# Kernel optimization log

Measured on AMD Instinct MI355X. Metric: run time of the kernel, lower is better.

Reference implementation:

```python
import jax, jax.numpy as jnp
import numpy as np

B, P, N, De, H, Do, T = 256, 48, 64, 64, 128, 64, 5
NR = N * (N - 1)
EPS = 1e-5


def _w(k, o, i):
    return jax.random.normal(k, (o, i), jnp.float32) * (1.0 / np.sqrt(i))


def setup_inputs() -> dict:
    key = jax.random.key(0)
    ks = jax.random.split(key, 12)
    x = jax.random.normal(ks[0], (B, P, N), jnp.float32)
    # fully-connected directed edges without self-loops (order matches itertools.product)
    idx = np.array([(r, s) for r in range(N) for s in range(N) if r != s], dtype=np.int32)
    receivers = jnp.asarray(idx[:, 0])
    senders = jnp.asarray(idx[:, 1])
    inp = {
        "x": x,
        "receivers": receivers,
        "senders": senders,
        "bn_gamma": jnp.ones((P,), jnp.float32),
        "bn_beta": jnp.zeros((P,), jnp.float32),
        "fr1_w": _w(ks[1], 4 * De, 2 * P), "fr1_b": jnp.zeros((4 * De,), jnp.float32),
        "fr2_w": _w(ks[2], 2 * De, 4 * De), "fr2_b": jnp.zeros((2 * De,), jnp.float32),
        "fr3_w": _w(ks[3], De, 2 * De), "fr3_b": jnp.zeros((De,), jnp.float32),
        "fo1_w": _w(ks[4], 2 * H, P + De), "fo1_b": jnp.zeros((2 * H,), jnp.float32),
        "fo2_w": _w(ks[5], H, 2 * H), "fo2_b": jnp.zeros((H,), jnp.float32),
        "fo3_w": _w(ks[6], Do, H), "fo3_b": jnp.zeros((Do,), jnp.float32),
        "fc1_w": _w(ks[7], 5 * T, Do), "fc1_b": jnp.zeros((5 * T,), jnp.float32),
        "fc2_w": _w(ks[8], 3 * T, 5 * T), "fc2_b": jnp.zeros((3 * T,), jnp.float32),
        "fc3_w": _w(ks[9], T, 3 * T), "fc3_b": jnp.zeros((T,), jnp.float32),
    }
    return inp


def _conv1(x, w, b):  # 1x1 Conv1d: x [B,Cin,L], w [Cout,Cin]
    return jnp.einsum('oi,bil->bol', w, x) + b[None, :, None]


def _forward(x, receivers, senders, bn_gamma, bn_beta,
             fr1_w, fr1_b, fr2_w, fr2_b, fr3_w, fr3_b,
             fo1_w, fo1_b, fo2_w, fo2_b, fo3_w, fo3_b,
             fc1_w, fc1_b, fc2_w, fc2_b, fc3_w, fc3_b):
    relu = jax.nn.relu
    # BatchNorm1d(P) in training mode: stats over (batch, length)
    mean = jnp.mean(x, axis=(0, 2), keepdims=True)
    var = jnp.var(x, axis=(0, 2), keepdims=True)
    xn = (x - mean) * jax.lax.rsqrt(var + EPS)
    xn = xn * bn_gamma[None, :, None] + bn_beta[None, :, None]
    # tmul(x, Rr)/tmul(x, Rs) are one-hot gathers along node axis -> [B, P, Nr]
    Orr = xn[:, :, receivers]
    Ors = xn[:, :, senders]
    Bmat = jnp.concatenate([Orr, Ors], axis=1)  # [B, 2P, Nr]
    Bmat = relu(_conv1(Bmat, fr1_w, fr1_b))
    Bmat = relu(_conv1(Bmat, fr2_w, fr2_b))
    E = relu(_conv1(Bmat, fr3_w, fr3_b))  # [B, De, Nr]
    # tmul(E, Rr^T) is scatter-add of edge features onto receiver nodes
    Ebar = jnp.zeros((x.shape[0], De, N), E.dtype).at[:, :, receivers].add(E)
    C = jnp.concatenate([xn, Ebar], axis=1)  # [B, P+De, N]
    C = relu(_conv1(C, fo1_w, fo1_b))
    C = relu(_conv1(C, fo2_w, fo2_b))
    O = relu(_conv1(C, fo3_w, fo3_b))  # [B, Do, N]
    Nsum = jnp.sum(O, axis=2)  # sum over constituents -> [B, Do]
    # fc_fixed1/2/3 applied with NO intermediate activations
    out = Nsum @ fc1_w.T + fc1_b
    out = out @ fc2_w.T + fc2_b
    out = out @ fc3_w.T + fc3_b
    return out


def reference(x, receivers, senders, bn_gamma, bn_beta,
              fr1_w, fr1_b, fr2_w, fr2_b, fr3_w, fr3_b,
              fo1_w, fo1_b, fo2_w, fo2_b, fo3_w, fo3_b,
              fc1_w, fc1_b, fc2_w, fc2_b, fc3_w, fc3_b):
    return _forward(x, receivers, senders, bn_gamma, bn_beta,
                    fr1_w, fr1_b, fr2_w, fr2_b, fr3_w, fr3_b,
                    fo1_w, fo1_b, fo2_w, fo2_b, fo3_w, fo3_b,
                    fc1_w, fc1_b, fc2_w, fc2_b, fc3_w, fc3_b)
```

## Files before the change

kernel.cpp:

```cpp
#include <hip/hip_runtime.h>
#include <hip/hip_bf16.h>

#define BB 256
#define PP 48
#define NN 64
#define EPSBN 1e-5f

typedef __attribute__((ext_vector_type(8))) short bf16x8;
typedef __attribute__((ext_vector_type(4))) float f32x4;

#define BIGO 0
#define S1SO 32768
#define S1RO 49152
#define F3LO 65536
#define A2WO 73728
#define XNTP 73728
#define B2LO 81408
#define REDO 81664
#define LDSE 81920

#define W_FR1R 0
#define W_FR1S 16384
#define W_FR2  32768
#define W_FR3  65536
#define W_FO1  73728
#define W_FO2  106496
#define W_FO3  139264
#define W_TOT  147456

union U8 { bf16x8 v; unsigned u[4]; };

__device__ __forceinline__ unsigned pku(float a, float b) {
    union { __hip_bfloat162 h; unsigned u; } cv;
    cv.h = __float22bfloat162_rn(make_float2(a, b));
    return cv.u;
}
__device__ __forceinline__ ushort f2b(float f) {
    union { float f; unsigned u; } a; a.f = f;
    unsigned u = a.u + 0x7FFFu + ((a.u >> 16) & 1u);
    return (ushort)(u >> 16);
}
__device__ __forceinline__ float loF(unsigned u) { union { unsigned x; float f; } c; c.x = u << 16; return c.f; }
__device__ __forceinline__ float hiF(unsigned u) { union { unsigned x; float f; } c; c.x = u & 0xffff0000u; return c.f; }

__device__ __forceinline__ int sidx(int row, int k, int kpad) {
    return row * kpad + ((((k >> 3) ^ (row & 7)) << 3) | (k & 7));
}
__device__ __forceinline__ bf16x8 ldfrag(const ushort* buf, int row, int k, int kpad) {
    return *(const bf16x8*)(buf + row * kpad + (((k >> 3) ^ (row & 7)) << 3));
}
__device__ __forceinline__ bf16x8 ldfrag40(const ushort* buf, int row, int k) {
    return *(const bf16x8*)(buf + row * 40 + k);
}
__device__ __forceinline__ f32x4 MFMA(bf16x8 a, bf16x8 b, f32x4 c) {
    return __builtin_amdgcn_mfma_f32_16x16x32_bf16(a, b, c, 0, 0, 0);
}
__device__ __forceinline__ void stAct(ushort* buf, int row, int c0, int kpad, f32x4 a, float4 bi) {
    uint2 o;
    o.x = pku(fmaxf(a[0] + bi.x, 0.f), fmaxf(a[1] + bi.y, 0.f));
    o.y = pku(fmaxf(a[2] + bi.z, 0.f), fmaxf(a[3] + bi.w, 0.f));
    *(uint2*)(buf + row * kpad + ((((c0 >> 3) ^ (row & 7)) << 3) | (c0 & 7))) = o;
}
__device__ __forceinline__ void stAct040(ushort* buf, int row, int c0, f32x4 a) {
    uint2 o;
    o.x = pku(fmaxf(a[0], 0.f), fmaxf(a[1], 0.f));
    o.y = pku(fmaxf(a[2], 0.f), fmaxf(a[3], 0.f));
    *(uint2*)(buf + row * 40 + c0) = o;
}
__device__ __forceinline__ void stRaw(ushort* buf, int row, int c0, int kpad, f32x4 a, float4 bi) {
    uint2 o;
    o.x = pku(a[0] + bi.x, a[1] + bi.y);
    o.y = pku(a[2] + bi.z, a[3] + bi.w);
    *(uint2*)(buf + row * kpad + ((((c0 >> 3) ^ (row & 7)) << 3) | (c0 & 7))) = o;
}

__global__ __launch_bounds__(256) void bn_stats_kernel(
    const float* __restrict__ x, const float* __restrict__ gamma,
    const float* __restrict__ beta, float* __restrict__ scale, float* __restrict__ bias)
{
    __shared__ float s_sum[256], s_sq[256];
    int p = blockIdx.x, t = threadIdx.x;
    float sum = 0.f, sq = 0.f;
    for (int i = t; i < BB * NN; i += 256) {
        int b = i >> 6, n = i & 63;
        float v = x[b * PP * NN + p * NN + n];
        sum += v; sq += v * v;
    }
    s_sum[t] = sum; s_sq[t] = sq;
    __syncthreads();
    for (int off = 128; off > 0; off >>= 1) {
        if (t < off) { s_sum[t] += s_sum[t + off]; s_sq[t] += s_sq[t + off]; }
        __syncthreads();
    }
    if (t == 0) {
        float inv = 1.f / (float)(BB * NN);
        float mean = s_sum[0] * inv;
        float var  = s_sq[0] * inv - mean * mean;
        float sc   = gamma[p] * rsqrtf(var + EPSBN);
        scale[p] = sc;
        bias[p]  = beta[p] - mean * sc;
    }
}

__global__ __launch_bounds__(512) void prep_kernel(
    const float* __restrict__ fr1_w, const float* __restrict__ fr2_w,
    const float* __restrict__ fr3_w, const float* __restrict__ fo1_w,
    const float* __restrict__ fo2_w, const float* __restrict__ fo3_w,
    ushort* __restrict__ wsw)
{
    int i = blockIdx.x * 512 + threadIdx.x;
    if (i >= W_TOT) return;
    float v; int off, row, k, kpad;
    if (i < 16384)        { row = i >> 6; k = i & 63; kpad = 64;  off = W_FR1R;
                            v = (k < PP) ? fr1_w[row * 96 + k] : 0.f; }
    else if (i < 32768)   { int j = i - 16384;  row = j >> 6; k = j & 63;  kpad = 64;  off = W_FR1S;
                            v = (k < PP) ? fr1_w[row * 96 + PP + k] : 0.f; }
    else if (i < 65536)   { int j = i - 32768;  row = j >> 8; k = j & 255; kpad = 256; off = W_FR2;
                            v = fr2_w[row * 256 + k]; }
    else if (i < 73728)   { int j = i - 65536;  row = j >> 7; k = j & 127; kpad = 128; off = W_FR3;
                            v = fr3_w[row * 128 + k]; }
    else if (i < 106496)  { int j = i - 73728;  row = j >> 7; k = j & 127; kpad = 128; off = W_FO1;
                            v = (k < 64) ? fo1_w[row * 112 + PP + k]
                              : (k < 112 ? fo1_w[row * 112 + (k - 64)] : 0.f); }
    else if (i < 139264)  { int j = i - 106496; row = j >> 8; k = j & 255; kpad = 256; off = W_FO2;
                            v = fo2_w[row * 256 + k]; }
    else                  { int j = i - 139264; row = j >> 7; k = j & 127; kpad = 128; off = W_FO3;
                            v = fo3_w[row * 128 + k]; }
    wsw[off + sidx(row, k, kpad)] = f2b(v);
}

__device__ __forceinline__ void wcopy(ushort* dst, const ushort* src, int n, int t) {
    for (int i = t * 8; i < n; i += 768 * 8)
        *(uint4*)(dst + i) = *(const uint4*)(src + i);
}

__global__ __launch_bounds__(768, 3) void meg_kernel(
    const float* __restrict__ x,
    const float* __restrict__ scl, const float* __restrict__ bia,
    const ushort* __restrict__ wsw,
    const float* __restrict__ fr1_b, const float* __restrict__ fr2_b,
    const float* __restrict__ fr3_b, const float* __restrict__ fo1_b,
    const float* __restrict__ fo2_b, const float* __restrict__ fo3_b,
    const float* __restrict__ fc1_w, const float* __restrict__ fc1_b,
    const float* __restrict__ fc2_w, const float* __restrict__ fc2_b,
    const float* __restrict__ fc3_w, const float* __restrict__ fc3_b,
    float* __restrict__ out)
{
    __shared__ __align__(16) ushort L[LDSE];

    int b = blockIdx.x, t = threadIdx.x;
    int w = t >> 6, l = t & 63, lx = l & 15, lq = l >> 4;

    for (int i = t; i < 4096; i += 768) {
        int n = i & 63, k = i >> 6;
        float v = (k < PP) ? x[b * PP * NN + k * NN + n] * scl[k] + bia[k] : 0.f;
        L[XNTP + sidx(n, k, 64)] = f2b(v);
    }
    wcopy(L + BIGO,         wsw + W_FR1R, 16384, t);
    wcopy(L + BIGO + 16384, wsw + W_FR1S, 16384, t);
    wcopy(L + F3LO,         wsw + W_FR3,  8192, t);
    if (t < 128) ((float*)(L + B2LO))[t] = fr2_b[t];
    __syncthreads();

    for (int mt = w; mt < 16; mt += 12) {
        f32x4 aR[4], aS[4];
#pragma unroll
        for (int nt = 0; nt < 4; ++nt) { aR[nt] = (f32x4){0.f,0.f,0.f,0.f}; aS[nt] = (f32x4){0.f,0.f,0.f,0.f}; }
#pragma unroll
        for (int ks = 0; ks < 2; ++ks) {
            bf16x8 AfR = ldfrag(L + BIGO,         mt * 16 + lx, ks * 32 + lq * 8, 64);
            bf16x8 AfS = ldfrag(L + BIGO + 16384, mt * 16 + lx, ks * 32 + lq * 8, 64);
#pragma unroll
            for (int nt = 0; nt < 4; ++nt) {
                bf16x8 Bf = ldfrag(L + XNTP, nt * 16 + lx, ks * 32 + lq * 8, 64);
                aR[nt] = MFMA(AfR, Bf, aR[nt]);
                aS[nt] = MFMA(AfS, Bf, aS[nt]);
            }
        }
        int ch0 = mt * 16 + lq * 4;
        float4 bi = *(const float4*)(fr1_b + ch0);
        float4 zb = make_float4(0.f, 0.f, 0.f, 0.f);
#pragma unroll
        for (int nt = 0; nt < 4; ++nt) {
            stRaw(L + S1RO, nt * 16 + lx, ch0, 256, aR[nt], bi);
            stRaw(L + S1SO, nt * 16 + lx, ch0, 256, aS[nt], zb);
        }
    }
    __syncthreads();

    wcopy(L + BIGO, wsw + W_FR2, 32768, t);
    float b3c[4];
#pragma unroll
    for (int n3 = 0; n3 < 4; ++n3) b3c[n3] = fr3_b[n3 * 16 + lx];
    __syncthreads();

    ushort* a2w = L + A2WO + w * 640;
    const float* b2L = (const float*)(L + B2LO);
#pragma unroll 1
    for (int r = w; r < 64; r += 12) {
        float part[4] = {0.f, 0.f, 0.f, 0.f};
#pragma unroll 1
        for (int p = 0; p < 2; ++p) {
            int eA = p * 32 + lx, eB = eA + 16;
            int sA = eA + (eA >= r);
            int sB = eB + (eB >= r); if (sB > 63) sB = 63;

            f32x4 acc2[8][2];
#pragma unroll
            for (int m = 0; m < 8; ++m) {
                float4 bv = *(const float4*)(b2L + m * 16 + lq * 4);
                f32x4 bi; bi[0] = bv.x; bi[1] = bv.y; bi[2] = bv.z; bi[3] = bv.w;
                acc2[m][0] = bi; acc2[m][1] = bi;
            }
#pragma unroll
            for (int ks = 0; ks < 8; ++ks) {
                int ko = ks * 32 + lq * 8;
                U8 fr, fa, fb;
                fr.v = ldfrag(L + S1RO, r,  ko, 256);
                fa.v = ldfrag(L + S1SO, sA, ko, 256);
                fb.v = ldfrag(L + S1SO, sB, ko, 256);
                U8 bA, bB;
#pragma unroll
                for (int jj = 0; jj < 4; ++jj) {
                    float r0 = loF(fr.u[jj]), r1 = hiF(fr.u[jj]);
                    bA.u[jj] = pku(fmaxf(r0 + loF(fa.u[jj]), 0.f), fmaxf(r1 + hiF(fa.u[jj]), 0.f));
                    bB.u[jj] = pku(fmaxf(r0 + loF(fb.u[jj]), 0.f), fmaxf(r1 + hiF(fb.u[jj]), 0.f));
                }
#pragma unroll
                for (int m = 0; m < 8; ++m) {
                    bf16x8 Af = ldfrag(L + BIGO, m * 16 + lx, ko, 256);
                    acc2[m][0] = MFMA(Af, bA.v, acc2[m][0]);
                    acc2[m][1] = MFMA(Af, bB.v, acc2[m][1]);
                }
            }
            f32x4 acc3[2][4];
#pragma unroll
            for (int cc = 0; cc < 2; ++cc)
#pragma unroll
                for (int n3 = 0; n3 < 4; ++n3) acc3[cc][n3] = (f32x4){0.f,0.f,0.f,0.f};
#pragma unroll
            for (int h = 0; h < 4; ++h) {
                bf16x8 bW[4];
#pragma unroll
                for (int n3 = 0; n3 < 4; ++n3)
                    bW[n3] = ldfrag(L + F3LO, n3 * 16 + lx, h * 32 + lq * 8, 128);
#pragma unroll
                for (int cc = 0; cc < 2; ++cc) {
                    stAct040(a2w, lx, lq * 4,      acc2[2 * h][cc]);
                    stAct040(a2w, lx, 16 + lq * 4, acc2[2 * h + 1][cc]);
                    bf16x8 af = ldfrag40(a2w, lx, lq * 8);
#pragma unroll
                    for (int n3 = 0; n3 < 4; ++n3)
                        acc3[cc][n3] = MFMA(af, bW[n3], acc3[cc][n3]);
                }
            }
#pragma unroll
            for (int cc = 0; cc < 2; ++cc) {
                bool mpad = (p == 1) && (cc == 1) && (lq == 3);
#pragma unroll
                for (int n3 = 0; n3 < 4; ++n3) {
                    float bv = b3c[n3];
                    float s = fmaxf(acc3[cc][n3][0] + bv, 0.f) + fmaxf(acc3[cc][n3][1] + bv, 0.f)
                            + fmaxf(acc3[cc][n3][2] + bv, 0.f);
                    float s3 = fmaxf(acc3[cc][n3][3] + bv, 0.f);
                    part[n3] += s + (mpad ? 0.f : s3);
                }
            }
        }
#pragma unroll
        for (int n3 = 0; n3 < 4; ++n3) {
            part[n3] += __shfl_xor(part[n3], 16, 64);
            part[n3] += __shfl_xor(part[n3], 32, 64);
        }
        if (lq == 0) {
#pragma unroll
            for (int n3 = 0; n3 < 4; ++n3)
                L[S1RO + sidx(r, n3 * 16 + lx, 256)] = f2b(part[n3]);
        }
    }
    __syncthreads();

    wcopy(L + BIGO, wsw + W_FO1, 32768, t);
    for (int i = t; i < 4096; i += 768) {
        int n = i & 63, k = i >> 6;
        float v = (k < PP) ? x[b * PP * NN + k * NN + n] * scl[k] + bia[k] : 0.f;
        L[S1RO + sidx(n, 64 + k, 256)] = f2b(v);
    }
    __syncthreads();

    for (int mt = w; mt < 16; mt += 12) {
        f32x4 accN[4];
#pragma unroll
        for (int nt = 0; nt < 4; ++nt) accN[nt] = (f32x4){0.f,0.f,0.f,0.f};
#pragma unroll
        for (int ks = 0; ks < 4; ++ks) {
            bf16x8 Af = ldfrag(L + BIGO, mt * 16 + lx, ks * 32 + lq * 8, 128);
#pragma unroll
            for (int nt = 0; nt < 4; ++nt) {
                bf16x8 Bf = ldfrag(L + S1RO, nt * 16 + lx, ks * 32 + lq * 8, 256);
                accN[nt] = MFMA(Af, Bf, accN[nt]);
            }
        }
        int ch0 = mt * 16 + lq * 4;
        float4 bi = *(const float4*)(fo1_b + ch0);
#pragma unroll
        for (int nt = 0; nt < 4; ++nt)
            stAct(L + S1SO, nt * 16 + lx, ch0, 256, accN[nt], bi);
    }
    __syncthreads();

    wcopy(L + BIGO, wsw + W_FO2, 32768, t);
    wcopy(L + S1RO, wsw + W_FO3, 8192, t);
    __syncthreads();

    if (w < 8) {
        f32x4 a2N[4];
#pragma unroll
        for (int nt = 0; nt < 4; ++nt) a2N[nt] = (f32x4){0.f,0.f,0.f,0.f};
#pragma unroll
        for (int ks = 0; ks < 8; ++ks) {
            bf16x8 Af = ldfrag(L + BIGO, w * 16 + lx, ks * 32 + lq * 8, 256);
#pragma unroll
            for (int nt = 0; nt < 4; ++nt) {
                bf16x8 Bf = ldfrag(L + S1SO, nt * 16 + lx, ks * 32 + lq * 8, 256);
                a2N[nt] = MFMA(Af, Bf, a2N[nt]);
            }
        }
        int ch0 = w * 16 + lq * 4;
        float4 bi = *(const float4*)(fo2_b + ch0);
#pragma unroll
        for (int nt = 0; nt < 4; ++nt)
            stAct(L + F3LO, nt * 16 + lx, ch0, 128, a2N[nt], bi);
    }
    __syncthreads();

    if (w < 4) {
        f32x4 a3N[4];
#pragma unroll
        for (int nt = 0; nt < 4; ++nt) a3N[nt] = (f32x4){0.f,0.f,0.f,0.f};
#pragma unroll
        for (int ks3 = 0; ks3 < 4; ++ks3) {
            bf16x8 Af = ldfrag(L + S1RO, 16 * w + lx, ks3 * 32 + lq * 8, 128);
#pragma unroll
            for (int nt = 0; nt < 4; ++nt) {
                bf16x8 Bf = ldfrag(L + F3LO, nt * 16 + lx, ks3 * 32 + lq * 8, 128);
                a3N[nt] = MFMA(Af, Bf, a3N[nt]);
            }
        }
        float4 b3 = *(const float4*)(fo3_b + 16 * w + lq * 4);
        float o0 = 0.f, o1 = 0.f, o2 = 0.f, o3 = 0.f;
#pragma unroll
        for (int nt = 0; nt < 4; ++nt) {
            o0 += fmaxf(a3N[nt][0] + b3.x, 0.f);
            o1 += fmaxf(a3N[nt][1] + b3.y, 0.f);
            o2 += fmaxf(a3N[nt][2] + b3.z, 0.f);
            o3 += fmaxf(a3N[nt][3] + b3.w, 0.f);
        }
#pragma unroll
        for (int off = 8; off >= 1; off >>= 1) {
            o0 += __shfl_xor(o0, off, 16);
            o1 += __shfl_xor(o1, off, 16);
            o2 += __shfl_xor(o2, off, 16);
            o3 += __shfl_xor(o3, off, 16);
        }
        if (lx == 0) {
            float* red = (float*)(L + REDO);
            *(float4*)&red[16 * w + lq * 4] = make_float4(o0, o1, o2, o3);
        }
    }
    __syncthreads();

    {
        float* red = (float*)(L + REDO);
        float* h1  = red + 64;
        float* h2  = red + 96;
        if (t < 25) {
            float s = fc1_b[t];
            for (int k = 0; k < 64; ++k) s += fc1_w[t * 64 + k] * red[k];
            h1[t] = s;
        }
        __syncthreads();
        if (t < 15) {
            float s = fc2_b[t];
            for (int k = 0; k < 25; ++k) s += fc2_w[t * 25 + k] * h1[k];
            h2[t] = s;
        }
        __syncthreads();
        if (t < 5) {
            float s = fc3_b[t];
            for (int k = 0; k < 15; ++k) s += fc3_w[t * 15 + k] * h2[k];
            out[b * 5 + t] = s;
        }
    }
}

extern "C" void kernel_launch(void* const* d_in, const int* in_sizes, int n_in,
                              void* d_out, int out_size, void* d_ws, size_t ws_size,
                              hipStream_t stream)
{
    const float* x        = (const float*)d_in[0];
    const float* bn_gamma = (const float*)d_in[3];
    const float* bn_beta  = (const float*)d_in[4];
    const float* fr1_w = (const float*)d_in[5];
    const float* fr1_b = (const float*)d_in[6];
    const float* fr2_w = (const float*)d_in[7];
    const float* fr2_b = (const float*)d_in[8];
    const float* fr3_w = (const float*)d_in[9];
    const float* fr3_b = (const float*)d_in[10];
    const float* fo1_w = (const float*)d_in[11];
    const float* fo1_b = (const float*)d_in[12];
    const float* fo2_w = (const float*)d_in[13];
    const float* fo2_b = (const float*)d_in[14];
    const float* fo3_w = (const float*)d_in[15];
    const float* fo3_b = (const float*)d_in[16];
    const float* fc1_w = (const float*)d_in[17];
    const float* fc1_b = (const float*)d_in[18];
    const float* fc2_w = (const float*)d_in[19];
    const float* fc2_b = (const float*)d_in[20];
    const float* fc3_w = (const float*)d_in[21];
    const float* fc3_b = (const float*)d_in[22];

    float* ws    = (float*)d_ws;
    float* scale = ws;
    float* bias  = ws + 64;
    ushort* wsw  = (ushort*)(ws + 128);
    float* out   = (float*)d_out;

    bn_stats_kernel<<<dim3(PP), dim3(256), 0, stream>>>(x, bn_gamma, bn_beta, scale, bias);
    prep_kernel<<<dim3(W_TOT / 512), dim3(512), 0, stream>>>(
        fr1_w, fr2_w, fr3_w, fo1_w, fo2_w, fo3_w, wsw);
    meg_kernel<<<dim3(BB), dim3(768), 0, stream>>>(
        x, scale, bias, wsw,
        fr1_b, fr2_b, fr3_b, fo1_b, fo2_b, fo3_b,
        fc1_w, fc1_b, fc2_w, fc2_b, fc3_w, fc3_b, out);
}
```

Baseline: 231.7 us.

## Precompute normalized bf16 swizzled input in prep kernel and parallelize FC tail

The batch-normalized, transposed, bf16-swizzled input is now produced once per batch element in the prep kernel and stored in the workspace. The main kernel pulls it in with vectorized 16-byte copies instead of doing strided fp32 gathers and conversion twice. The fo1 GEMM reads its x-part straight from that buffer rather than first copying it into the S1RO region. BN stats now runs 1024 threads per block, and the final three tiny FC layers use wave-level shuffle reductions instead of a few serial threads, at the cost of an extra 2 MB workspace round-trip.

```diff
diff --git a/kernel.cpp b/kernel.cpp
--- a/kernel.cpp
+++ b/kernel.cpp
@@ -27,6 +27,8 @@
 #define W_FO2  106496
 #define W_FO3  139264
 #define W_TOT  147456
+#define W_XNT  147456
+#define W_ALL  (W_XNT + BB * 4096)
 
 union U8 { bf16x8 v; unsigned u[4]; };
 
@@ -74,21 +76,21 @@
     *(uint2*)(buf + row * kpad + ((((c0 >> 3) ^ (row & 7)) << 3) | (c0 & 7))) = o;
 }
 
-__global__ __launch_bounds__(256) void bn_stats_kernel(
+__global__ __launch_bounds__(1024) void bn_stats_kernel(
     const float* __restrict__ x, const float* __restrict__ gamma,
     const float* __restrict__ beta, float* __restrict__ scale, float* __restrict__ bias)
 {
-    __shared__ float s_sum[256], s_sq[256];
+    __shared__ float s_sum[1024], s_sq[1024];
     int p = blockIdx.x, t = threadIdx.x;
     float sum = 0.f, sq = 0.f;
-    for (int i = t; i < BB * NN; i += 256) {
+    for (int i = t; i < BB * NN; i += 1024) {
         int b = i >> 6, n = i & 63;
         float v = x[b * PP * NN + p * NN + n];
         sum += v; sq += v * v;
     }
     s_sum[t] = sum; s_sq[t] = sq;
     __syncthreads();
-    for (int off = 128; off > 0; off >>= 1) {
+    for (int off = 512; off > 0; off >>= 1) {
         if (t < off) { s_sum[t] += s_sum[t + off]; s_sq[t] += s_sq[t + off]; }
         __syncthreads();
     }
@@ -106,10 +108,18 @@
     const float* __restrict__ fr1_w, const float* __restrict__ fr2_w,
     const float* __restrict__ fr3_w, const float* __restrict__ fo1_w,
     const float* __restrict__ fo2_w, const float* __restrict__ fo3_w,
-    ushort* __restrict__ wsw)
+    const float* __restrict__ x, const float* __restrict__ scale,
+    const float* __restrict__ bias, ushort* __restrict__ wsw)
 {
     int i = blockIdx.x * 512 + threadIdx.x;
-    if (i >= W_TOT) return;
+    if (i >= W_ALL) return;
+    if (i >= W_TOT) {
+        int j = i - W_XNT;
+        int b = j >> 12, nk = j & 4095, n = nk & 63, k = nk >> 6;
+        float v = (k < PP) ? x[b * PP * NN + k * NN + n] * scale[k] + bias[k] : 0.f;
+        wsw[W_XNT + (b << 12) + sidx(n, k, 64)] = f2b(v);
+        return;
+    }
     float v; int off, row, k, kpad;
     if (i < 16384)        { row = i >> 6; k = i & 63; kpad = 64;  off = W_FR1R;
                             v = (k < PP) ? fr1_w[row * 96 + k] : 0.f; }
@@ -135,8 +145,6 @@
 }
 
 __global__ __launch_bounds__(768, 3) void meg_kernel(
-    const float* __restrict__ x,
-    const float* __restrict__ scl, const float* __restrict__ bia,
     const ushort* __restrict__ wsw,
     const float* __restrict__ fr1_b, const float* __restrict__ fr2_b,
     const float* __restrict__ fr3_b, const float* __restrict__ fo1_b,
@@ -151,11 +159,7 @@
     int b = blockIdx.x, t = threadIdx.x;
     int w = t >> 6, l = t & 63, lx = l & 15, lq = l >> 4;
 
-    for (int i = t; i < 4096; i += 768) {
-        int n = i & 63, k = i >> 6;
-        float v = (k < PP) ? x[b * PP * NN + k * NN + n] * scl[k] + bia[k] : 0.f;
-        L[XNTP + sidx(n, k, 64)] = f2b(v);
-    }
+    wcopy(L + XNTP,         wsw + W_XNT + (b << 12), 4096, t);
     wcopy(L + BIGO,         wsw + W_FR1R, 16384, t);
     wcopy(L + BIGO + 16384, wsw + W_FR1S, 16384, t);
     wcopy(L + F3LO,         wsw + W_FR3,  8192, t);
@@ -281,11 +285,7 @@
     __syncthreads();
 
     wcopy(L + BIGO, wsw + W_FO1, 32768, t);
-    for (int i = t; i < 4096; i += 768) {
-        int n = i & 63, k = i >> 6;
-        float v = (k < PP) ? x[b * PP * NN + k * NN + n] * scl[k] + bia[k] : 0.f;
-        L[S1RO + sidx(n, 64 + k, 256)] = f2b(v);
-    }
+    wcopy(L + XNTP, wsw + W_XNT + (b << 12), 4096, t);
     __syncthreads();
 
     for (int mt = w; mt < 16; mt += 12) {
@@ -297,7 +297,8 @@
             bf16x8 Af = ldfrag(L + BIGO, mt * 16 + lx, ks * 32 + lq * 8, 128);
 #pragma unroll
             for (int nt = 0; nt < 4; ++nt) {
-                bf16x8 Bf = ldfrag(L + S1RO, nt * 16 + lx, ks * 32 + lq * 8, 256);
+                bf16x8 Bf = (ks < 2) ? ldfrag(L + S1RO, nt * 16 + lx, ks * 32 + lq * 8, 256)
+                                     : ldfrag(L + XNTP, nt * 16 + lx, (ks - 2) * 32 + lq * 8, 64);
                 accN[nt] = MFMA(Af, Bf, accN[nt]);
             }
         }
@@ -374,22 +375,25 @@
         float* red = (float*)(L + REDO);
         float* h1  = red + 64;
         float* h2  = red + 96;
-        if (t < 25) {
-            float s = fc1_b[t];
-            for (int k = 0; k < 64; ++k) s += fc1_w[t * 64 + k] * red[k];
-            h1[t] = s;
+        for (int o = w; o < 25; o += 12) {
+            float v = fc1_w[o * 64 + l] * red[l];
+#pragma unroll
+            for (int off = 32; off >= 1; off >>= 1) v += __shfl_xor(v, off, 64);
+            if (l == 0) h1[o] = v + fc1_b[o];
         }
         __syncthreads();
-        if (t < 15) {
-            float s = fc2_b[t];
-            for (int k = 0; k < 25; ++k) s += fc2_w[t * 25 + k] * h1[k];
-            h2[t] = s;
+        for (int o = w; o < 15; o += 12) {
+            float v = (l < 25) ? fc2_w[o * 25 + l] * h1[l] : 0.f;
+#pragma unroll
+            for (int off = 32; off >= 1; off >>= 1) v += __shfl_xor(v, off, 64);
+            if (l == 0) h2[o] = v + fc2_b[o];
         }
         __syncthreads();
-        if (t < 5) {
-            float s = fc3_b[t];
-            for (int k = 0; k < 15; ++k) s += fc3_w[t * 15 + k] * h2[k];
-            out[b * 5 + t] = s;
+        if (w < 5) {
+            float v = (l < 15) ? fc3_w[w * 15 + l] * h2[l] : 0.f;
+#pragma unroll
+            for (int off = 32; off >= 1; off >>= 1) v += __shfl_xor(v, off, 64);
+            if (l == 0) out[b * 5 + w] = v + fc3_b[w];
         }
     }
 }
@@ -426,11 +430,11 @@
     ushort* wsw  = (ushort*)(ws + 128);
     float* out   = (float*)d_out;
 
-    bn_stats_kernel<<<dim3(PP), dim3(256), 0, stream>>>(x, bn_gamma, bn_beta, scale, bias);
-    prep_kernel<<<dim3(W_TOT / 512), dim3(512), 0, stream>>>(
-        fr1_w, fr2_w, fr3_w, fo1_w, fo2_w, fo3_w, wsw);
+    bn_stats_kernel<<<dim3(PP), dim3(1024), 0, stream>>>(x, bn_gamma, bn_beta, scale, bias);
+    prep_kernel<<<dim3(W_ALL / 512), dim3(512), 0, stream>>>(
+        fr1_w, fr2_w, fr3_w, fo1_w, fo2_w, fo3_w, x, scale, bias, wsw);
     meg_kernel<<<dim3(BB), dim3(768), 0, stream>>>(
-        x, scale, bias, wsw,
+        wsw,
         fr1_b, fr2_b, fr3_b, fo1_b, fo2_b, fo3_b,
         fc1_w, fc1_b, fc2_w, fc2_b, fc3_w, fc3_b, out);
 }
```

Result: faster. 225.2 us (-2.8%).
